# Performance work log

Measured on AMD Instinct MI355X. Metric: run time of the kernel, lower is better.

The kernel has to match this reference:

```python
import jax, jax.numpy as jnp
from jax import lax
import numpy as np

N = 4096      # graph nodes
K = 16        # sampled local-neighborhood size (2-hop proxy)
T = 16        # number of templates
NT = 16       # nodes per template
D = 128       # node feature dim
OUTER = 3     # proximal / mirror-descent iterations
INNER = 5     # sinkhorn iterations per outer step
EPS_REL = 0.1 # entropic reg relative to cost range
TINY = 1e-16


def setup_inputs() -> dict:
    key = jax.random.key(0)
    ks = jax.random.split(key, 8)
    x = jax.random.normal(ks[0], (N, D), jnp.float32)
    adj = (jax.random.uniform(ks[1], (N, N)) < 0.004).astype(jnp.float32)
    adj = jnp.maximum(adj, adj.T)
    neighbors = jax.random.randint(ks[2], (N, K), 0, N, dtype=jnp.int32)
    templates = (jax.random.randint(ks[3], (T, NT, NT), 0, 2).astype(jnp.float32)
                 + 0.01 * jax.random.normal(ks[4], (T, NT, NT), jnp.float32))
    templates_features = 0.0012 + 0.02 * jax.random.normal(ks[5], (T, NT, D), jnp.float32)
    q0 = jax.random.uniform(ks[6], (T, NT), jnp.float32)
    alpha0 = jnp.zeros((1,), jnp.float32)
    return {"x": x, "adj": adj, "neighbors": neighbors, "templates": templates,
            "templates_features": templates_features, "q0": q0, "alpha0": alpha0}


def _ltfgw(x, adj, neighbors, templates, templates_features, q0, alpha0):
    n, d = x.shape
    t, nt, _ = templates.shape
    k1 = neighbors.shape[1] + 1
    nb = jnp.concatenate([jnp.arange(n, dtype=neighbors.dtype)[:, None], neighbors], axis=1)  # [N,K1]
    Fi = x[nb]                                    # [N,K1,D] local node features
    C1 = adj[nb[:, :, None], nb[:, None, :]]      # [N,K1,K1] local structure
    C2 = templates                                # [T,NT,NT]
    alpha = jax.nn.sigmoid(alpha0[0])
    q = jax.nn.softmax(q0, axis=1)                # [T,NT] template node weights
    p = jnp.full((k1,), 1.0 / k1, x.dtype)        # uniform local weights
    # squared-euclidean feature cost M: [N,T,K1,NT]
    M = (jnp.sum(Fi**2, -1)[:, None, :, None]
         + jnp.sum(templates_features**2, -1)[None, :, None, :]
         - 2.0 * jnp.einsum('nkd,tmd->ntkm', Fi, templates_features))
    # constant part of squared-loss GW cost
    cC = (jnp.einsum('nij,j->ni', C1**2, p)[:, None, :, None]
          + jnp.einsum('tm,tlm->tl', q, C2**2)[None, :, None, :])
    G0 = jnp.broadcast_to(p[None, None, :, None] * q[None, :, None, :], (n, t, k1, nt))

    def outer_step(G, _):
        gw_grad = cC - 2.0 * jnp.einsum('nij,ntjm,tlm->ntil', C1, G, C2)
        grad = (1.0 - alpha) * M + alpha * gw_grad
        lo = jnp.min(grad, axis=(-2, -1), keepdims=True)
        hi = jnp.max(grad, axis=(-2, -1), keepdims=True)
        eps = EPS_REL * (hi - lo) + TINY
        Kmat = jnp.exp(-(grad - lo) / eps)        # per-(n,t) shift leaves plan invariant

        def sink(uv, _):
            u, v = uv
            u = p[None, None, :] / jnp.maximum(jnp.einsum('ntkm,ntm->ntk', Kmat, v), TINY)
            v = q[None] / jnp.maximum(jnp.einsum('ntkm,ntk->ntm', Kmat, u), TINY)
            return (u, v), None

        u0 = jnp.ones((n, t, k1), x.dtype)
        v0 = jnp.ones((n, t, nt), x.dtype)
        (u, v), _ = lax.scan(sink, (u0, v0), None, length=INNER)
        return u[..., None] * Kmat * v[..., None, :], None

    G, _ = lax.scan(outer_step, G0, None, length=OUTER)
    gw = cC - 2.0 * jnp.einsum('nij,ntjm,tlm->ntil', C1, G, C2)
    # fused GW distance of every node's local graph to every template: [N,T]
    return jnp.sum(((1.0 - alpha) * M + alpha * gw) * G, axis=(-2, -1))


def reference(x, adj, neighbors, templates, templates_features, q0, alpha0):
    return _ltfgw(x, adj, neighbors, templates, templates_features, q0, alpha0)
```

## Files before the change

### kernel.cpp

```cpp
#include <hip/hip_runtime.h>
#include <math.h>


#define NN 4096
#define KNB 16
#define K1 17
#define C1STRIDE 20
#define C1NODE 340
#define TSTR 296
#define TINYF 1e-16f

typedef const __attribute__((address_space(4))) float* c4fp;
typedef const __attribute__((address_space(4))) int*   c4ip;
__device__ __forceinline__ float sload(const float* p){ return *(c4fp)(unsigned long long)p; }
__device__ __forceinline__ int   sloadi(const int* p) { return *(c4ip)(unsigned long long)p; }

template<int CTRL>
__device__ __forceinline__ float dppmov(float x) {
  return __int_as_float(
      __builtin_amdgcn_update_dpp(0, __float_as_int(x), CTRL, 0xF, 0xF, true));
}
__device__ __forceinline__ float xor4v(float x) {
  return dppmov<0x1B>(dppmov<0x141>(x));
}
__device__ __forceinline__ float rsum16(float x) {
  x += dppmov<0xB1>(x); x += dppmov<0x4E>(x);
  x += xor4v(x);        x += dppmov<0x128>(x);
  return x;
}
__device__ __forceinline__ float rmin16(float x) {
  x = fminf(x, dppmov<0xB1>(x)); x = fminf(x, dppmov<0x4E>(x));
  x = fminf(x, xor4v(x));        x = fminf(x, dppmov<0x128>(x));
  return x;
}
__device__ __forceinline__ float rmax16(float x) {
  x = fmaxf(x, dppmov<0xB1>(x)); x = fmaxf(x, dppmov<0x4E>(x));
  x = fmaxf(x, xor4v(x));        x = fmaxf(x, dppmov<0x128>(x));
  return x;
}
__device__ __forceinline__ float rcpn(float x) {
  float r = __builtin_amdgcn_rcpf(x);
  return r * (2.f - x * r);
}

#define WSTEP(C, R) { g = dppmov<C>(g); acc = fmaf(g, c2reg[R], acc); }
#define WALK15() \
  WSTEP(0xB1,1)  WSTEP(0x1B,2)  WSTEP(0xB1,3)  WSTEP(0x141,4) \
  WSTEP(0xB1,5)  WSTEP(0x1B,6)  WSTEP(0xB1,7)  WSTEP(0x140,8) \
  WSTEP(0xB1,9)  WSTEP(0x1B,10) WSTEP(0xB1,11) WSTEP(0x141,12) \
  WSTEP(0xB1,13) WSTEP(0x1B,14) WSTEP(0xB1,15)

#define PG_GEMM  256
#define PG_XSQ   (PG_GEMM + 1024)
#define PG_SCAL  PG_XSQ
#define PG_C1    (PG_SCAL + 1)
#define PG_TOT   (PG_C1 + 4096)

__global__ __launch_bounds__(256) void prep_combined(
    const float* __restrict__ x, const float* __restrict__ adj,
    const int* __restrict__ neighbors, const float* __restrict__ templates_,
    const float* __restrict__ tf, const float* __restrict__ q0,
    const float* __restrict__ alpha0,
    float* __restrict__ P, float* __restrict__ C1ws, float* __restrict__ xsq,
    float* __restrict__ tfsq, float* __restrict__ qmat, float* __restrict__ cq,
    float* __restrict__ walpha) {
  __shared__ __align__(16) float smem[2 * 64 * 68];
  const int b = blockIdx.x, tid = threadIdx.x;

  if (b < PG_GEMM) {
    float (*As)[68] = (float (*)[68])smem;
    float (*Bs)[68] = (float (*)[68])(smem + 64 * 68);
    int tx = tid & 15, ty = tid >> 4;
    int r0 = (b & 63) * 64, c0 = (b >> 6) * 64;
    float acc[4][4] = {};
    for (int h = 0; h < 2; ++h) {
      __syncthreads();
#pragma unroll
      for (int q = 0; q < 4; ++q) {
        int f = tid + 256*q;
        int row = f >> 4, d4 = (f & 15) << 2;
        float4 a = *(const float4*)&x[(r0+row)*128 + h*64 + d4];
        As[d4+0][row]=a.x; As[d4+1][row]=a.y; As[d4+2][row]=a.z; As[d4+3][row]=a.w;
        float4 bb = *(const float4*)&tf[(c0+row)*128 + h*64 + d4];
        Bs[d4+0][row]=bb.x; Bs[d4+1][row]=bb.y; Bs[d4+2][row]=bb.z; Bs[d4+3][row]=bb.w;
      }
      __syncthreads();
#pragma unroll
      for (int d = 0; d < 64; ++d) {
        float4 a = *(const float4*)&As[d][ty*4];
        float4 bb = *(const float4*)&Bs[d][tx*4];
        float av[4]={a.x,a.y,a.z,a.w}, bv[4]={bb.x,bb.y,bb.z,bb.w};
#pragma unroll
        for (int i = 0; i < 4; ++i)
#pragma unroll
          for (int j = 0; j < 4; ++j) acc[i][j] = fmaf(av[i], bv[j], acc[i][j]);
      }
    }
#pragma unroll
    for (int i = 0; i < 4; ++i) {
      float4 o; o.x=acc[i][0]; o.y=acc[i][1]; o.z=acc[i][2]; o.w=acc[i][3];
      *(float4*)&P[(r0 + ty*4 + i)*256 + c0 + tx*4] = o;
    }
    return;
  }

  if (b < PG_XSQ) {
    int n = (b - PG_GEMM)*4 + (tid >> 6), lane = tid & 63;
    float2 v = *(const float2*)&x[n*128 + lane*2];
    float s = fmaf(v.x, v.x, v.y*v.y);
    s += __shfl_xor(s,1); s += __shfl_xor(s,2);  s += __shfl_xor(s,4);
    s += __shfl_xor(s,8); s += __shfl_xor(s,16); s += __shfl_xor(s,32);
    if (lane == 0) xsq[n] = s;
    return;
  }

  if (b == PG_SCAL) {
    int t = tid >> 4, l = tid & 15;
    if (tid == 0) walpha[0] = 1.f / (1.f + expf(-alpha0[0]));
    float qr[16]; float mx = -3.0e38f;
#pragma unroll
    for (int m = 0; m < 16; ++m) { qr[m] = q0[t*16+m]; mx = fmaxf(mx, qr[m]); }
    float s = 0.f;
#pragma unroll
    for (int m = 0; m < 16; ++m) { qr[m] = expf(qr[m]-mx); s += qr[m]; }
    float inv = 1.f / s;
    qmat[tid] = qr[l] * inv;
    float c = 0.f;
#pragma unroll
    for (int m = 0; m < 16; ++m) {
      float c2 = templates_[t*256 + l*16 + m];
      c = fmaf(qr[m]*inv, c2*c2, c);
    }
    cq[tid] = c;
    float ts = 0.f;
#pragma unroll
    for (int dq = 0; dq < 32; ++dq) {
      float4 v = *(const float4*)&tf[tid*128 + dq*4];
      ts = fmaf(v.x,v.x,ts); ts = fmaf(v.y,v.y,ts);
      ts = fmaf(v.z,v.z,ts); ts = fmaf(v.w,v.w,ts);
    }
    tfsq[tid] = ts;
    return;
  }

  {
    int n = b - PG_C1;
    int*   nbs  = (int*)smem;
    float* c1sh = smem + 32;
    if (tid < K1) nbs[tid] = (tid == 0) ? n : neighbors[n*KNB + tid - 1];
    __syncthreads();
    for (int e = tid; e < 289; e += 256) {
      int i = e / 17, j = e % 17;
      float v = adj[nbs[i]*NN + nbs[j]];
      C1ws[n*C1NODE + i*C1STRIDE + j] = v;
      c1sh[e] = v;
    }
    __syncthreads();
    bool nz = false;
    if (tid < K1) {
      float s = 0.f;
#pragma unroll
      for (int j = 0; j < K1; ++j) {
        float v = c1sh[tid*17 + j];
        s = fmaf(v, v, s); nz |= (v != 0.f);
      }
      C1ws[n*C1NODE + tid*C1STRIDE + 17] = s * (1.f/17.f);
    }
    unsigned long long bal = __ballot(nz);
    if (tid == 0)
      ((int*)C1ws)[n*C1NODE + 18] = (int)(bal & 0x1FFFF);
  }
}

__global__ __launch_bounds__(256, 2) void ltfgw_main(
    const float* __restrict__ P, const float* __restrict__ C1ws,
    const float* __restrict__ xsq, const float* __restrict__ tfsq,
    const float* __restrict__ qmat, const float* __restrict__ cq,
    const float* __restrict__ walpha, const int* __restrict__ neighbors,
    const float* __restrict__ templates_, float* __restrict__ out) {
  __shared__ __align__(16) float Ksh[16 * TSTR];
  __shared__ __align__(16) float Ush[256];
  __shared__ __align__(16) float Vsh[256];

  const int tid = threadIdx.x;
  const int t = tid >> 4, l = tid & 15;
  const int n = blockIdx.x;

  const float alpha = sload(walpha);
  const float oma = 1.f - alpha;
  const float na2 = -2.f * alpha;
  const int mask = sloadi((const int*)C1ws + n*C1NODE + 18);

  int nbk[K1];
  nbk[0] = n;
#pragma unroll
  for (int k = 1; k < K1; ++k) nbk[k] = sloadi(neighbors + n*KNB + (k-1));

  const float tfsq_l = tfsq[tid];
  const float cq_l   = cq[tid];
  const float q_l    = qmat[tid];

  float Mcol[K1];
#pragma unroll
  for (int k = 0; k < K1; ++k) {
    float xs  = sload(xsq + nbk[k]);
    float cc1 = sload(C1ws + n*C1NODE + k*C1STRIDE + 17);
    float pv  = P[nbk[k]*256 + tid];
    Mcol[k] = oma * (xs + tfsq_l - 2.f*pv) + alpha * (cc1 + cq_l);
  }

  float c2reg[16];
#pragma unroll
  for (int r = 0; r < 16; ++r)
    c2reg[r] = na2 * templates_[t*256 + l*16 + (l ^ r)];

  float Gcol[K1];
#pragma unroll
  for (int j = 0; j < K1; ++j) Gcol[j] = (1.f/17.f) * q_l;

  const int tb = t * TSTR;
  float ur[16], u16 = 0.f, vm = 1.f;

#pragma unroll 1
  for (int outer = 0; outer < 3; ++outer) {
    float Kc[K1];
    float lo = 3.0e38f, hi = -3.0e38f;
#pragma unroll
    for (int i = 0; i < K1; ++i) {
      float gr = Mcol[i];
      if (mask & (1 << i)) {
        const float* c1r = C1ws + n*C1NODE + i*C1STRIDE;
        float s = 0.f;
#pragma unroll
        for (int j = 0; j < K1; ++j) s = fmaf(sload(c1r + j), Gcol[j], s);
        float g = s, acc = s * c2reg[0];
        WALK15()
        gr += acc;
      }
      Kc[i] = gr;
      lo = fminf(lo, gr); hi = fmaxf(hi, gr);
    }
    lo = rmin16(lo); hi = rmax16(hi);
    float eps = 0.1f * (hi - lo) + TINYF;
    float sc = 1.4426950408889634f * __builtin_amdgcn_rcpf(eps);
    float nsc = -sc, losc = lo * sc;
#pragma unroll
    for (int i = 0; i < K1; ++i) {
      Kc[i] = __builtin_amdgcn_exp2f(fmaf(Kc[i], nsc, losc));
      Ksh[tb + i*17 + l] = Kc[i];
    }
    float Krow[16];
#pragma unroll
    for (int jq = 0; jq < 4; ++jq) {
      float4 v = *(const float4*)&Ksh[tb + l*17 + jq*4];
      Krow[jq*4+0]=v.x; Krow[jq*4+1]=v.y; Krow[jq*4+2]=v.z; Krow[jq*4+3]=v.w;
    }

    float vlane = 1.f;
    Vsh[tid] = 1.f;
#pragma unroll 1
    for (int it = 0; it < 5; ++it) {
      float vr[16];
#pragma unroll
      for (int q = 0; q < 4; ++q) {
        float4 v = *(const float4*)&Vsh[t*16 + q*4];
        vr[q*4+0]=v.x; vr[q*4+1]=v.y; vr[q*4+2]=v.z; vr[q*4+3]=v.w;
      }
      float w = 0.f;
#pragma unroll
      for (int j = 0; j < 16; ++j) w = fmaf(Krow[j], vr[j], w);
      float w16 = rsum16(Kc[16] * vlane);
      float um = (1.f/17.f) * rcpn(fmaxf(w,   TINYF));
      u16      = (1.f/17.f) * rcpn(fmaxf(w16, TINYF));
      Ush[tid] = um;
#pragma unroll
      for (int q = 0; q < 4; ++q) {
        float4 v = *(const float4*)&Ush[t*16 + q*4];
        ur[q*4+0]=v.x; ur[q*4+1]=v.y; ur[q*4+2]=v.z; ur[q*4+3]=v.w;
      }
      float sg = u16 * Kc[16];
#pragma unroll
      for (int k = 0; k < 16; ++k) sg = fmaf(ur[k], Kc[k], sg);
      vlane = q_l * rcpn(fmaxf(sg, TINYF));
      Vsh[tid] = vlane;
    }
    vm = vlane;
#pragma unroll
    for (int k = 0; k < 16; ++k) Gcol[k] = ur[k] * Kc[k] * vm;
    Gcol[16] = u16 * Kc[16] * vm;
  }

  float acc1 = 0.f;
#pragma unroll
  for (int i = 0; i < K1; ++i) acc1 = fmaf(Mcol[i], Gcol[i], acc1);
#pragma unroll
  for (int i = 0; i < K1; ++i) {
    if (mask & (1 << i)) {
      const float* c1r = C1ws + n*C1NODE + i*C1STRIDE;
      float s = 0.f;
#pragma unroll
      for (int j = 0; j < K1; ++j) s = fmaf(sload(c1r + j), Gcol[j], s);
      float g = s, acc = s * c2reg[0];
      WALK15()
      acc1 = fmaf(acc, Gcol[i], acc1);
    }
  }
  float accout = rsum16(acc1);
  if (l == 0) out[n*16 + t] = accout;
}

extern "C" void kernel_launch(void* const* d_in, const int* in_sizes, int n_in,
                              void* d_out, int out_size, void* d_ws, size_t ws_size,
                              hipStream_t stream) {
  const float* x          = (const float*)d_in[0];
  const float* adj        = (const float*)d_in[1];
  const int*   neighbors  = (const int*)  d_in[2];
  const float* templates_ = (const float*)d_in[3];
  const float* tfeat      = (const float*)d_in[4];
  const float* q0         = (const float*)d_in[5];
  const float* alpha0     = (const float*)d_in[6];
  float* out = (float*)d_out;

  float* ws     = (float*)d_ws;
  float* P      = ws;
  float* C1ws   = P + 4096*256;
  float* xsq    = C1ws + 4096*C1NODE;
  float* tfsq   = xsq + 4096;
  float* qmat   = tfsq + 256;
  float* cq     = qmat + 256;
  float* walpha = cq + 256;

  hipLaunchKernelGGL(prep_combined, dim3(PG_TOT), dim3(256), 0, stream,
                     x, adj, neighbors, templates_, tfeat, q0, alpha0,
                     P, C1ws, xsq, tfsq, qmat, cq, walpha);
  hipLaunchKernelGGL(ltfgw_main, dim3(4096), dim3(256), 0, stream,
                     P, C1ws, xsq, tfsq, qmat, cq, walpha, neighbors,
                     templates_, out);
}
```

Before: 181.9 us.

## Pack adjacency into bitmasks and derive local structure in main kernel

```diff
diff --git a/kernel.cpp b/kernel.cpp
--- a/kernel.cpp
+++ b/kernel.cpp
@@ -5,8 +5,6 @@
 #define NN 4096
 #define KNB 16
 #define K1 17
-#define C1STRIDE 20
-#define C1NODE 340
 #define TSTR 296
 #define TINYF 1e-16f
 
@@ -53,15 +51,16 @@
 #define PG_GEMM  256
 #define PG_XSQ   (PG_GEMM + 1024)
 #define PG_SCAL  PG_XSQ
-#define PG_C1    (PG_SCAL + 1)
-#define PG_TOT   (PG_C1 + 4096)
+#define PG_ADJ   (PG_SCAL + 1)
+#define PG_TOT   (PG_ADJ + 4096)
 
 __global__ __launch_bounds__(256) void prep_combined(
     const float* __restrict__ x, const float* __restrict__ adj,
     const int* __restrict__ neighbors, const float* __restrict__ templates_,
     const float* __restrict__ tf, const float* __restrict__ q0,
     const float* __restrict__ alpha0,
-    float* __restrict__ P, float* __restrict__ C1ws, float* __restrict__ xsq,
+    float* __restrict__ P, unsigned* __restrict__ adjbits,
+    float* __restrict__ xsq,
     float* __restrict__ tfsq, float* __restrict__ qmat, float* __restrict__ cq,
     float* __restrict__ walpha) {
   __shared__ __align__(16) float smem[2 * 64 * 68];
@@ -144,36 +143,25 @@
   }
 
   {
-    int n = b - PG_C1;
-    int*   nbs  = (int*)smem;
-    float* c1sh = smem + 32;
-    if (tid < K1) nbs[tid] = (tid == 0) ? n : neighbors[n*KNB + tid - 1];
-    __syncthreads();
-    for (int e = tid; e < 289; e += 256) {
-      int i = e / 17, j = e % 17;
-      float v = adj[nbs[i]*NN + nbs[j]];
-      C1ws[n*C1NODE + i*C1STRIDE + j] = v;
-      c1sh[e] = v;
-    }
-    __syncthreads();
-    bool nz = false;
-    if (tid < K1) {
-      float s = 0.f;
-#pragma unroll
-      for (int j = 0; j < K1; ++j) {
-        float v = c1sh[tid*17 + j];
-        s = fmaf(v, v, s); nz |= (v != 0.f);
-      }
-      C1ws[n*C1NODE + tid*C1STRIDE + 17] = s * (1.f/17.f);
-    }
-    unsigned long long bal = __ballot(nz);
-    if (tid == 0)
-      ((int*)C1ws)[n*C1NODE + 18] = (int)(bal & 0x1FFFF);
+    int row = b - PG_ADJ;
+    const float4* ap = (const float4*)&adj[(long long)row * NN];
+    unsigned m = 0;
+#pragma unroll
+    for (int q = 0; q < 4; ++q) {
+      float4 v = ap[tid*4 + q];
+      m |= (unsigned)(v.x != 0.f) << (q*4 + 0);
+      m |= (unsigned)(v.y != 0.f) << (q*4 + 1);
+      m |= (unsigned)(v.z != 0.f) << (q*4 + 2);
+      m |= (unsigned)(v.w != 0.f) << (q*4 + 3);
+    }
+    unsigned other = (unsigned)__shfl_xor((int)m, 1);
+    if ((tid & 1) == 0)
+      adjbits[row*128 + (tid >> 1)] = m | (other << 16);
   }
 }
 
 __global__ __launch_bounds__(256, 2) void ltfgw_main(
-    const float* __restrict__ P, const float* __restrict__ C1ws,
+    const float* __restrict__ P, const unsigned* __restrict__ adjbits,
     const float* __restrict__ xsq, const float* __restrict__ tfsq,
     const float* __restrict__ qmat, const float* __restrict__ cq,
     const float* __restrict__ walpha, const int* __restrict__ neighbors,
@@ -181,20 +169,37 @@
   __shared__ __align__(16) float Ksh[16 * TSTR];
   __shared__ __align__(16) float Ush[256];
   __shared__ __align__(16) float Vsh[256];
+  __shared__ int nb_sh[20];
+  __shared__ int rm_sh[20];
 
   const int tid = threadIdx.x;
   const int t = tid >> 4, l = tid & 15;
   const int n = blockIdx.x;
 
+  if (tid < K1) {
+    nb_sh[tid] = (tid == 0) ? n : neighbors[n*KNB + tid - 1];
+    rm_sh[tid] = 0;
+  }
+  __syncthreads();
+  for (unsigned e = tid; e < 289; e += 256) {
+    unsigned i = e / 17u, j = e % 17u;
+    int ni = nb_sh[i], nj = nb_sh[j];
+    unsigned w = adjbits[ni*128 + (nj >> 5)];
+    if ((w >> (nj & 31)) & 1u) atomicOr(&rm_sh[i], 1 << j);
+  }
+  __syncthreads();
+
+  int rm[K1];
+  int nbk[K1];
+#pragma unroll
+  for (int k = 0; k < K1; ++k) {
+    rm[k]  = __builtin_amdgcn_readfirstlane(rm_sh[k]);
+    nbk[k] = __builtin_amdgcn_readfirstlane(nb_sh[k]);
+  }
+
   const float alpha = sload(walpha);
   const float oma = 1.f - alpha;
   const float na2 = -2.f * alpha;
-  const int mask = sloadi((const int*)C1ws + n*C1NODE + 18);
-
-  int nbk[K1];
-  nbk[0] = n;
-#pragma unroll
-  for (int k = 1; k < K1; ++k) nbk[k] = sloadi(neighbors + n*KNB + (k-1));
 
   const float tfsq_l = tfsq[tid];
   const float cq_l   = cq[tid];
@@ -204,7 +209,7 @@
 #pragma unroll
   for (int k = 0; k < K1; ++k) {
     float xs  = sload(xsq + nbk[k]);
-    float cc1 = sload(C1ws + n*C1NODE + k*C1STRIDE + 17);
+    float cc1 = (float)__popc((unsigned)rm[k]) * (1.f/17.f);
     float pv  = P[nbk[k]*256 + tid];
     Mcol[k] = oma * (xs + tfsq_l - 2.f*pv) + alpha * (cc1 + cq_l);
   }
@@ -228,11 +233,11 @@
 #pragma unroll
     for (int i = 0; i < K1; ++i) {
       float gr = Mcol[i];
-      if (mask & (1 << i)) {
-        const float* c1r = C1ws + n*C1NODE + i*C1STRIDE;
+      if (rm[i]) {
         float s = 0.f;
 #pragma unroll
-        for (int j = 0; j < K1; ++j) s = fmaf(sload(c1r + j), Gcol[j], s);
+        for (int j = 0; j < K1; ++j)
+          if (rm[i] & (1 << j)) s += Gcol[j];
         float g = s, acc = s * c2reg[0];
         WALK15()
         gr += acc;
@@ -295,11 +300,11 @@
   for (int i = 0; i < K1; ++i) acc1 = fmaf(Mcol[i], Gcol[i], acc1);
 #pragma unroll
   for (int i = 0; i < K1; ++i) {
-    if (mask & (1 << i)) {
-      const float* c1r = C1ws + n*C1NODE + i*C1STRIDE;
+    if (rm[i]) {
       float s = 0.f;
 #pragma unroll
-      for (int j = 0; j < K1; ++j) s = fmaf(sload(c1r + j), Gcol[j], s);
+      for (int j = 0; j < K1; ++j)
+        if (rm[i] & (1 << j)) s += Gcol[j];
       float g = s, acc = s * c2reg[0];
       WALK15()
       acc1 = fmaf(acc, Gcol[i], acc1);
@@ -321,19 +326,19 @@
   const float* alpha0     = (const float*)d_in[6];
   float* out = (float*)d_out;
 
-  float* ws     = (float*)d_ws;
-  float* P      = ws;
-  float* C1ws   = P + 4096*256;
-  float* xsq    = C1ws + 4096*C1NODE;
-  float* tfsq   = xsq + 4096;
-  float* qmat   = tfsq + 256;
-  float* cq     = qmat + 256;
-  float* walpha = cq + 256;
+  float* ws        = (float*)d_ws;
+  float* P         = ws;
+  unsigned* adjbits = (unsigned*)(P + 4096*256);
+  float* xsq       = (float*)(adjbits + 4096*128);
+  float* tfsq      = xsq + 4096;
+  float* qmat      = tfsq + 256;
+  float* cq        = qmat + 256;
+  float* walpha    = cq + 256;
 
   hipLaunchKernelGGL(prep_combined, dim3(PG_TOT), dim3(256), 0, stream,
                      x, adj, neighbors, templates_, tfeat, q0, alpha0,
-                     P, C1ws, xsq, tfsq, qmat, cq, walpha);
+                     P, adjbits, xsq, tfsq, qmat, cq, walpha);
   hipLaunchKernelGGL(ltfgw_main, dim3(4096), dim3(256), 0, stream,
-                     P, C1ws, xsq, tfsq, qmat, cq, walpha, neighbors,
+                     P, adjbits, xsq, tfsq, qmat, cq, walpha, neighbors,
                      templates_, out);
 }
```

After: 194.5 us. 1.07x slower.
